# Kernel tuning notes

Hardware: AMD Instinct MI355X
Metric: run time of the kernel (lower is better)

## Reference

```python
import jax, jax.numpy as jnp
import numpy as np

B, C, H, W = 32, 384, 28, 28
E, HID, K = 4, 384, 2  # HID = hidden_features(1536) // num_experts(4)


def setup_inputs() -> dict:
    key = jax.random.key(0)
    ks = jax.random.split(key, 5)
    x = jax.random.normal(ks[0], (B, C, H, W), jnp.float32)
    gate_w = jax.random.normal(ks[1], (C, E), jnp.float32) * 0.02
    gate_b = jnp.zeros((E,), jnp.float32)
    w1 = jax.random.normal(ks[2], (E, HID, C), jnp.float32) * 0.02
    b1 = jnp.zeros((E, HID), jnp.float32)
    w2 = jax.random.normal(ks[3], (E, C, HID), jnp.float32) * 0.02
    b2 = jnp.zeros((E, C), jnp.float32)
    return {"x": x, "gate_w": gate_w, "gate_b": gate_b,
            "w1": w1, "b1": b1, "w2": w2, "b2": b2}


def reference(x, gate_w, gate_b, w1, b1, w2, b2):
    b, c, h, w = x.shape
    e = gate_b.shape[0]
    # per-token gating: tokens are spatial positions in NHWC order
    x_flat = x.transpose(0, 2, 3, 1).reshape(-1, c)          # [N, C], N = B*H*W
    scores = jax.nn.softmax(x_flat @ gate_w + gate_b, -1)    # [N, E]
    top_v, top_i = jax.lax.top_k(scores, K)                  # [N, K]
    top_w = jax.nn.softmax(top_v, -1)                        # [N, K] renormalized
    # weight map per top-k slot: [K, B, H, W]
    wmap = top_w.T.reshape(K, b, h, w)
    # faithful to torch loop: expert i contributes at slot k iff ANY token routed
    # to it at slot k; the weight applied is the UNMASKED slot-k weight map.
    present = (top_i[:, :, None] == jnp.arange(e)[None, None, :]).any(0)  # [K, E]
    coef = jnp.einsum('ke,kbhw->ebhw', present.astype(x.dtype), wmap)     # [E, B, H, W]
    # dense per-expert 1x1-conv MLP over the FULL tensor (as in the source)
    hdn = jax.nn.relu(jnp.einsum('bchw,edc->ebdhw', x, w1)
                      + b1[:, None, :, None, None])          # [E, B, HID, H, W]
    y = jnp.einsum('ebdhw,eod->ebohw', hdn, w2) + b2[:, None, :, None, None]
    out = jnp.einsum('ebohw,ebhw->bohw', y, coef)            # [B, C, H, W]
    return out
```

## Files before the change

### kernel.cpp

```cpp
#include <hip/hip_runtime.h>
#include <hip/hip_bf16.h>
#include <stdint.h>

#define B_DIM 32
#define C_DIM 384
#define HW_DIM 784
#define E_DIM 4
#define HID_DIM 384
#define NTOK (B_DIM * HW_DIM)
#define NH (E_DIM * HID_DIM)

using short8 = __attribute__((ext_vector_type(8))) short;
using f32x4  = __attribute__((ext_vector_type(4))) float;
typedef unsigned short ushort_t;

__device__ __forceinline__ ushort_t f2bf(float f) {
  __hip_bfloat16 h = __float2bfloat16(f);
  return __builtin_bit_cast(ushort_t, h);
}

__device__ __forceinline__ void gload_lds16(const void* g, void* l) {
  __builtin_amdgcn_global_load_lds(
      (const __attribute__((address_space(1))) unsigned int*)g,
      (__attribute__((address_space(3))) unsigned int*)l, 16, 0, 0);
}

__global__ __launch_bounds__(256) void prep_kernel(
    const float* __restrict__ w1, const float* __restrict__ w2,
    ushort_t* __restrict__ W1b, ushort_t* __restrict__ W2b,
    unsigned int* __restrict__ present) {
  int i = blockIdx.x * 256 + threadIdx.x;
  if (i == 0) *present = 0u;
  if (i < NH * C_DIM) {
    W1b[i] = f2bf(w1[i]);
    int o = i / NH;
    int r = i - o * NH;
    int e = r / HID_DIM;
    int k = r - e * HID_DIM;
    W2b[i] = f2bf(w2[((size_t)e * C_DIM + o) * HID_DIM + k]);
  }
}

__global__ __launch_bounds__(256) void gate_kernel(
    const float* __restrict__ x, const float* __restrict__ gw,
    const float* __restrict__ gb, ushort_t* __restrict__ xb,
    float* __restrict__ topw, unsigned int* __restrict__ present) {
  __shared__ __align__(16) ushort_t lxs[64][392];
  __shared__ float pscore[4][64][4];
  __shared__ unsigned int pmask;
  const int b = blockIdx.x;
  const int p0 = blockIdx.y * 64;
  const int cnt = min(64, HW_DIM - p0);
  const int tid = threadIdx.x;
  const int cg = tid >> 6, tl = tid & 63;
  if (tid == 0) pmask = 0u;
  float a0 = 0.f, a1 = 0.f, a2 = 0.f, a3 = 0.f;
  const bool valid = tl < cnt;
  if (valid) {
    const float* xp = x + (size_t)b * C_DIM * HW_DIM + p0 + tl;
    for (int c = cg; c < C_DIM; c += 4) {
      const float v = xp[(size_t)c * HW_DIM];
      lxs[tl][c] = f2bf(v);
      const float4 g = *(const float4*)&gw[c * 4];
      a0 += v * g.x; a1 += v * g.y; a2 += v * g.z; a3 += v * g.w;
    }
  }
  pscore[cg][tl][0] = a0; pscore[cg][tl][1] = a1;
  pscore[cg][tl][2] = a2; pscore[cg][tl][3] = a3;
  __syncthreads();
  if (cg == 0 && valid) {
    float z[4];
#pragma unroll
    for (int e = 0; e < 4; e++)
      z[e] = pscore[0][tl][e] + pscore[1][tl][e] + pscore[2][tl][e] +
             pscore[3][tl][e] + gb[e];
    const float mx = fmaxf(fmaxf(z[0], z[1]), fmaxf(z[2], z[3]));
    float s[4]; float sum = 0.f;
#pragma unroll
    for (int e = 0; e < 4; e++) { s[e] = __expf(z[e] - mx); sum += s[e]; }
    const float inv = 1.f / sum;
#pragma unroll
    for (int e = 0; e < 4; e++) s[e] *= inv;
    int e0 = 0; float v0 = s[0];
#pragma unroll
    for (int e = 1; e < 4; e++) if (s[e] > v0) { v0 = s[e]; e0 = e; }
    int e1 = -1; float v1 = -1.f;
#pragma unroll
    for (int e = 0; e < 4; e++) if (e != e0 && s[e] > v1) { v1 = s[e]; e1 = e; }
    const float r = __expf(v1 - v0);
    const float w0 = 1.f / (1.f + r);
    const int m = b * HW_DIM + p0 + tl;
    topw[m * 2] = w0;
    topw[m * 2 + 1] = 1.f - w0;
    atomicOr(&pmask, (1u << e0) | (1u << (4 + e1)));
  }
  __syncthreads();
  if (tid == 0) atomicOr(present, pmask);
  const int nchunk = cnt * 48;
  for (int ci = tid; ci < nchunk; ci += 256) {
    const int row = ci / 48, c8 = ci - row * 48;
    short8 v = *(const short8*)&lxs[row][c8 * 8];
    *(short8*)&xb[(size_t)(b * HW_DIM + p0 + row) * C_DIM + c8 * 8] = v;
  }
}

template <int KDIM, int EPI>
__global__ __launch_bounds__(256, 2) void gemm_p4(
    const ushort_t* __restrict__ A, const ushort_t* __restrict__ Bw,
    const float* __restrict__ bias, const float* __restrict__ topw,
    const unsigned int* __restrict__ presentp,
    ushort_t* __restrict__ hOut, float* __restrict__ outp) {
  constexpr int BM = 128, BN = 128, BK = 32;
  constexpr int KT = KDIM / BK;
  constexpr int NTN = (EPI == 0 ? NH / BN : C_DIM / BN);
  constexpr int ASZ = BM * BK;
  __shared__ ushort_t smem[8 * ASZ];

  const int nwg = NTN * (NTOK / BM);
  const int orig = blockIdx.x;
  const int xcd = orig & 7;
  const int qq = nwg >> 3, rr = nwg & 7;
  const int wg = (xcd < rr ? xcd * (qq + 1) : rr * (qq + 1) + (xcd - rr) * qq)
               + (orig >> 3);
  const int mt = wg / NTN, nt = wg % NTN;
  const int m0 = mt * BM, n0 = nt * BN;

  const int tid = threadIdx.x;
  const int lane = tid & 63;
  const int wid = tid >> 6;
  const int wm = wid >> 1, wn = wid & 1;
  const int lanel = lane & 15, laneq = lane >> 4;

  auto stage = [&](int t) {
    ushort_t* dstA = smem + (t & 3) * ASZ;
    ushort_t* dstB = smem + 4 * ASZ + (t & 3) * ASZ;
    const int kb = t * BK;
#pragma unroll
    for (int li = 0; li < 2; ++li) {
      const int P = (li * 256 + tid) * 16;
      const int row = P >> 6;
      const int cb = (P & 63) ^ (((row >> 1) & 3) << 4);
      gload_lds16(&A[(size_t)(m0 + row) * KDIM + kb + (cb >> 1)],
                  (char*)dstA + P);
    }
#pragma unroll
    for (int li = 0; li < 2; ++li) {
      const int P = (li * 256 + tid) * 16;
      const int row = P >> 6;
      const int cb = (P & 63) ^ (((row >> 1) & 3) << 4);
      gload_lds16(&Bw[(size_t)(n0 + row) * KDIM + kb + (cb >> 1)],
                  (char*)dstB + P);
    }
  };

  f32x4 acc[4][4] = {};
  const int cbr = (laneq * 16) ^ (((lanel >> 1) & 3) << 4);

  stage(0);
  stage(1);
  stage(2);
  for (int t = 0; t < KT; ++t) {
    if (t + 3 < KT) stage(t + 3);
    const int ahead = min(3, KT - 1 - t);
    if (ahead == 3)      asm volatile("s_waitcnt vmcnt(12)" ::: "memory");
    else if (ahead == 2) asm volatile("s_waitcnt vmcnt(8)" ::: "memory");
    else if (ahead == 1) asm volatile("s_waitcnt vmcnt(4)" ::: "memory");
    else                 asm volatile("s_waitcnt vmcnt(0)" ::: "memory");
    __builtin_amdgcn_sched_barrier(0);
    __builtin_amdgcn_s_barrier();
    __builtin_amdgcn_sched_barrier(0);
    const char* Ab =
        (const char*)(smem + (t & 3) * ASZ) + (wm * 64 + lanel) * 64;
    const char* Bb =
        (const char*)(smem + 4 * ASZ + (t & 3) * ASZ) + (wn * 64 + lanel) * 64;
    short8 av[4], bv[4];
#pragma unroll
    for (int i = 0; i < 4; ++i) av[i] = *(const short8*)(Ab + i * 1024 + cbr);
#pragma unroll
    for (int j = 0; j < 4; ++j) bv[j] = *(const short8*)(Bb + j * 1024 + cbr);
    __builtin_amdgcn_s_setprio(1);
#pragma unroll
    for (int i = 0; i < 4; ++i)
#pragma unroll
      for (int j = 0; j < 4; ++j)
        acc[i][j] = __builtin_amdgcn_mfma_f32_16x16x32_bf16(
            av[i], bv[j], acc[i][j], 0, 0, 0);
    __builtin_amdgcn_s_setprio(0);
    __builtin_amdgcn_sched_barrier(0);
    __builtin_amdgcn_s_barrier();
    __builtin_amdgcn_sched_barrier(0);
  }

  const unsigned int pm = *presentp;
  if constexpr (EPI == 0) {
    __syncthreads();
    ushort_t* tr = smem;
    const int e = n0 / HID_DIM;
    const float P0 = (float)((pm >> e) & 1u);
    const float P1 = (float)((pm >> (4 + e)) & 1u);
#pragma unroll
    for (int mi = 0; mi < 4; ++mi) {
      const int r0 = wm * 64 + mi * 16 + laneq * 4;
      const int mg = m0 + r0;
      const float4 t0 = *(const float4*)&topw[mg * 2];
      const float4 t1 = *(const float4*)&topw[mg * 2 + 4];
      const float cj[4] = {P0 * t0.x + P1 * t0.y, P0 * t0.z + P1 * t0.w,
                           P0 * t1.x + P1 * t1.y, P0 * t1.z + P1 * t1.w};
#pragma unroll
      for (int ni = 0; ni < 4; ++ni) {
        const int cl = wn * 64 + ni * 16 + lanel;
        const float bvv = bias[n0 + cl];
#pragma unroll
        for (int j = 0; j < 4; ++j) {
          float v = fmaxf(acc[mi][ni][j] + bvv, 0.f);
          tr[(r0 + j) * 128 + cl] = f2bf(cj[j] * v);
        }
      }
    }
    __syncthreads();
#pragma unroll
    for (int it = 0; it < 8; ++it) {
      const int c = it * 256 + tid;
      const int row = c >> 4, cr = c & 15;
      *(short8*)&hOut[(size_t)(m0 + row) * NH + n0 + cr * 8] =
          *(const short8*)&tr[row * 128 + cr * 8];
    }
  } else {
    float B0[4], B1[4];
#pragma unroll
    for (int ni = 0; ni < 4; ++ni) {
      const int o = n0 + wn * 64 + ni * 16 + lanel;
      float s0 = 0.f, s1 = 0.f;
#pragma unroll
      for (int e2 = 0; e2 < 4; ++e2) {
        const float bb = bias[e2 * C_DIM + o];
        s0 += (float)((pm >> e2) & 1u) * bb;
        s1 += (float)((pm >> (4 + e2)) & 1u) * bb;
      }
      B0[ni] = s0; B1[ni] = s1;
    }
#pragma unroll
    for (int mi = 0; mi < 4; ++mi) {
      const int mg = m0 + wm * 64 + mi * 16 + laneq * 4;
      const float4 t0 = *(const float4*)&topw[mg * 2];
      const float4 t1 = *(const float4*)&topw[mg * 2 + 4];
      const int bb2 = mg / HW_DIM;
      const int p = mg - bb2 * HW_DIM;
#pragma unroll
      for (int ni = 0; ni < 4; ++ni) {
        const int o = n0 + wn * 64 + ni * 16 + lanel;
        float4 v;
        v.x = acc[mi][ni][0] + t0.x * B0[ni] + t0.y * B1[ni];
        v.y = acc[mi][ni][1] + t0.z * B0[ni] + t0.w * B1[ni];
        v.z = acc[mi][ni][2] + t1.x * B0[ni] + t1.y * B1[ni];
        v.w = acc[mi][ni][3] + t1.z * B0[ni] + t1.w * B1[ni];
        *(float4*)&outp[((size_t)bb2 * C_DIM + o) * HW_DIM + p] = v;
      }
    }
  }
}

extern "C" void kernel_launch(void* const* d_in, const int* in_sizes, int n_in,
                              void* d_out, int out_size, void* d_ws, size_t ws_size,
                              hipStream_t stream) {
  const float* x  = (const float*)d_in[0];
  const float* gw = (const float*)d_in[1];
  const float* gb = (const float*)d_in[2];
  const float* w1 = (const float*)d_in[3];
  const float* b1 = (const float*)d_in[4];
  const float* w2 = (const float*)d_in[5];
  const float* b2 = (const float*)d_in[6];
  float* out = (float*)d_out;

  char* ws = (char*)d_ws;
  ushort_t* xb = (ushort_t*)ws;   ws += (size_t)NTOK * C_DIM * 2;
  ushort_t* hdnS = (ushort_t*)ws; ws += (size_t)NTOK * NH * 2;
  ushort_t* W1b = (ushort_t*)ws;  ws += (size_t)NH * C_DIM * 2;
  ushort_t* W2b = (ushort_t*)ws;  ws += (size_t)C_DIM * NH * 2;
  float* topw = (float*)ws;       ws += (size_t)NTOK * 2 * 4;
  unsigned int* present = (unsigned int*)ws;

  prep_kernel<<<dim3((NH * C_DIM) / 256), dim3(256), 0, stream>>>(
      w1, w2, W1b, W2b, present);
  gate_kernel<<<dim3(B_DIM, 13), dim3(256), 0, stream>>>(
      x, gw, gb, xb, topw, present);
  gemm_p4<C_DIM, 0>
      <<<dim3((NTOK / 128) * (NH / 128)), dim3(256), 0, stream>>>(
          xb, W1b, b1, topw, present, hdnS, nullptr);
  gemm_p4<NH, 1>
      <<<dim3((NTOK / 128) * (C_DIM / 128)), dim3(256), 0, stream>>>(
          hdnS, W2b, b2, topw, present, nullptr, out);
}
```

Measured before the change: 137.8 us.

## Enlarge GEMM M-tile to 256 with triple-buffered LDS pipeline

Doubles the GEMM block tile along M from 128 to 256 rows, so each wave holds 8x4 MFMA accumulators and reuses each B fragment across twice as many rows. To fit the larger A tile in LDS, the prefetch depth drops from four buffers to three, with adjusted vmcnt waits. The EPI==0 epilogue now stages the output through LDS in two halves. The goal is higher arithmetic intensity per LDS and global load, paid for with more accumulator registers, possibly lower occupancy, shallower prefetch and fewer workgroups (NTOK/256 = 98 M-tiles).

```diff
diff --git a/kernel.cpp b/kernel.cpp
--- a/kernel.cpp
+++ b/kernel.cpp
@@ -105,16 +105,17 @@
 }
 
 template <int KDIM, int EPI>
-__global__ __launch_bounds__(256, 2) void gemm_p4(
+__global__ __launch_bounds__(256, 2) void gemm_v9(
     const ushort_t* __restrict__ A, const ushort_t* __restrict__ Bw,
     const float* __restrict__ bias, const float* __restrict__ topw,
     const unsigned int* __restrict__ presentp,
     ushort_t* __restrict__ hOut, float* __restrict__ outp) {
-  constexpr int BM = 128, BN = 128, BK = 32;
+  constexpr int BM = 256, BN = 128, BK = 32;
   constexpr int KT = KDIM / BK;
   constexpr int NTN = (EPI == 0 ? NH / BN : C_DIM / BN);
   constexpr int ASZ = BM * BK;
-  __shared__ ushort_t smem[8 * ASZ];
+  constexpr int BSZ = BN * BK;
+  __shared__ ushort_t smem[3 * ASZ + 3 * BSZ];
 
   const int nwg = NTN * (NTOK / BM);
   const int orig = blockIdx.x;
@@ -132,11 +133,12 @@
   const int lanel = lane & 15, laneq = lane >> 4;
 
   auto stage = [&](int t) {
-    ushort_t* dstA = smem + (t & 3) * ASZ;
-    ushort_t* dstB = smem + 4 * ASZ + (t & 3) * ASZ;
+    const int buf = t % 3;
+    ushort_t* dstA = smem + buf * ASZ;
+    ushort_t* dstB = smem + 3 * ASZ + buf * BSZ;
     const int kb = t * BK;
 #pragma unroll
-    for (int li = 0; li < 2; ++li) {
+    for (int li = 0; li < 4; ++li) {
       const int P = (li * 256 + tid) * 16;
       const int row = P >> 6;
       const int cb = (P & 63) ^ (((row >> 1) & 3) << 4);
@@ -153,34 +155,33 @@
     }
   };
 
-  f32x4 acc[4][4] = {};
+  f32x4 acc[8][4] = {};
   const int cbr = (laneq * 16) ^ (((lanel >> 1) & 3) << 4);
 
   stage(0);
   stage(1);
-  stage(2);
   for (int t = 0; t < KT; ++t) {
-    if (t + 3 < KT) stage(t + 3);
-    const int ahead = min(3, KT - 1 - t);
-    if (ahead == 3)      asm volatile("s_waitcnt vmcnt(12)" ::: "memory");
-    else if (ahead == 2) asm volatile("s_waitcnt vmcnt(8)" ::: "memory");
-    else if (ahead == 1) asm volatile("s_waitcnt vmcnt(4)" ::: "memory");
+    if (t + 2 < KT) stage(t + 2);
+    const int ahead = min(2, KT - 1 - t);
+    if (ahead == 2)      asm volatile("s_waitcnt vmcnt(12)" ::: "memory");
+    else if (ahead == 1) asm volatile("s_waitcnt vmcnt(6)" ::: "memory");
     else                 asm volatile("s_waitcnt vmcnt(0)" ::: "memory");
     __builtin_amdgcn_sched_barrier(0);
     __builtin_amdgcn_s_barrier();
     __builtin_amdgcn_sched_barrier(0);
+    const int buf = t % 3;
     const char* Ab =
-        (const char*)(smem + (t & 3) * ASZ) + (wm * 64 + lanel) * 64;
+        (const char*)(smem + buf * ASZ) + (wm * 128 + lanel) * 64;
     const char* Bb =
-        (const char*)(smem + 4 * ASZ + (t & 3) * ASZ) + (wn * 64 + lanel) * 64;
-    short8 av[4], bv[4];
-#pragma unroll
-    for (int i = 0; i < 4; ++i) av[i] = *(const short8*)(Ab + i * 1024 + cbr);
+        (const char*)(smem + 3 * ASZ + buf * BSZ) + (wn * 64 + lanel) * 64;
+    short8 av[8], bv[4];
+#pragma unroll
+    for (int i = 0; i < 8; ++i) av[i] = *(const short8*)(Ab + i * 1024 + cbr);
 #pragma unroll
     for (int j = 0; j < 4; ++j) bv[j] = *(const short8*)(Bb + j * 1024 + cbr);
     __builtin_amdgcn_s_setprio(1);
 #pragma unroll
-    for (int i = 0; i < 4; ++i)
+    for (int i = 0; i < 8; ++i)
 #pragma unroll
       for (int j = 0; j < 4; ++j)
         acc[i][j] = __builtin_amdgcn_mfma_f32_16x16x32_bf16(
@@ -199,31 +200,37 @@
     const float P0 = (float)((pm >> e) & 1u);
     const float P1 = (float)((pm >> (4 + e)) & 1u);
 #pragma unroll
-    for (int mi = 0; mi < 4; ++mi) {
-      const int r0 = wm * 64 + mi * 16 + laneq * 4;
-      const int mg = m0 + r0;
-      const float4 t0 = *(const float4*)&topw[mg * 2];
-      const float4 t1 = *(const float4*)&topw[mg * 2 + 4];
-      const float cj[4] = {P0 * t0.x + P1 * t0.y, P0 * t0.z + P1 * t0.w,
-                           P0 * t1.x + P1 * t1.y, P0 * t1.z + P1 * t1.w};
-#pragma unroll
-      for (int ni = 0; ni < 4; ++ni) {
-        const int cl = wn * 64 + ni * 16 + lanel;
-        const float bvv = bias[n0 + cl];
-#pragma unroll
-        for (int j = 0; j < 4; ++j) {
-          float v = fmaxf(acc[mi][ni][j] + bvv, 0.f);
-          tr[(r0 + j) * 128 + cl] = f2bf(cj[j] * v);
+    for (int s = 0; s < 2; ++s) {
+      if (wm == s) {
+#pragma unroll
+        for (int mi = 0; mi < 8; ++mi) {
+          const int rloc = mi * 16 + laneq * 4;
+          const int mg = m0 + s * 128 + rloc;
+          const float4 t0 = *(const float4*)&topw[mg * 2];
+          const float4 t1 = *(const float4*)&topw[mg * 2 + 4];
+          const float cj[4] = {P0 * t0.x + P1 * t0.y, P0 * t0.z + P1 * t0.w,
+                               P0 * t1.x + P1 * t1.y, P0 * t1.z + P1 * t1.w};
+#pragma unroll
+          for (int ni = 0; ni < 4; ++ni) {
+            const int cl = wn * 64 + ni * 16 + lanel;
+            const float bvv = bias[n0 + cl];
+#pragma unroll
+            for (int j = 0; j < 4; ++j) {
+              float v = fmaxf(acc[mi][ni][j] + bvv, 0.f);
+              tr[(rloc + j) * 128 + cl] = f2bf(cj[j] * v);
+            }
+          }
         }
       }
-    }
-    __syncthreads();
-#pragma unroll
-    for (int it = 0; it < 8; ++it) {
-      const int c = it * 256 + tid;
-      const int row = c >> 4, cr = c & 15;
-      *(short8*)&hOut[(size_t)(m0 + row) * NH + n0 + cr * 8] =
-          *(const short8*)&tr[row * 128 + cr * 8];
+      __syncthreads();
+#pragma unroll
+      for (int it = 0; it < 8; ++it) {
+        const int c = it * 256 + tid;
+        const int row = c >> 4, cr = c & 15;
+        *(short8*)&hOut[(size_t)(m0 + s * 128 + row) * NH + n0 + cr * 8] =
+            *(const short8*)&tr[row * 128 + cr * 8];
+      }
+      __syncthreads();
     }
   } else {
     float B0[4], B1[4];
@@ -240,8 +247,8 @@
       B0[ni] = s0; B1[ni] = s1;
     }
 #pragma unroll
-    for (int mi = 0; mi < 4; ++mi) {
-      const int mg = m0 + wm * 64 + mi * 16 + laneq * 4;
+    for (int mi = 0; mi < 8; ++mi) {
+      const int mg = m0 + wm * 128 + mi * 16 + laneq * 4;
       const float4 t0 = *(const float4*)&topw[mg * 2];
       const float4 t1 = *(const float4*)&topw[mg * 2 + 4];
       const int bb2 = mg / HW_DIM;
@@ -284,10 +291,10 @@
       w1, w2, W1b, W2b, present);
   gate_kernel<<<dim3(B_DIM, 13), dim3(256), 0, stream>>>(
       x, gw, gb, xb, topw, present);
-  gemm_p4<C_DIM, 0>
-      <<<dim3((NTOK / 128) * (NH / 128)), dim3(256), 0, stream>>>(
+  gemm_v9<C_DIM, 0>
+      <<<dim3((NTOK / 256) * (NH / 128)), dim3(256), 0, stream>>>(
           xb, W1b, b1, topw, present, hdnS, nullptr);
-  gemm_p4<NH, 1>
-      <<<dim3((NTOK / 128) * (C_DIM / 128)), dim3(256), 0, stream>>>(
+  gemm_v9<NH, 1>
+      <<<dim3((NTOK / 256) * (C_DIM / 128)), dim3(256), 0, stream>>>(
           hdnS, W2b, b2, topw, present, nullptr, out);
 }
```

After: 148.3 us. +7.6%, slower.
